# Optimization experiments

Measured on AMD Instinct MI355X. Metric: run time of the kernel, lower is better.

## Reference

```python
import jax, jax.numpy as jnp
import numpy as np

N, E, IN_DIM, HID, OUT, H = 50000, 800000, 128, 96, 96, 4
C1, C2 = HID // H, OUT // H
EPS = 1e-5

def _lin(key, out_f, in_f):
    kw, kb = jax.random.split(key)
    s = 1.0 / np.sqrt(in_f)
    W = jax.random.uniform(kw, (out_f, in_f), jnp.float32, -s, s)
    b = jax.random.uniform(kb, (out_f,), jnp.float32, -s, s)
    return W, b

def setup_inputs() -> dict:
    key = jax.random.key(0)
    ks = jax.random.split(key, 16)
    x = jax.random.normal(ks[0], (N, IN_DIM), jnp.float32)
    edge_index = jax.random.randint(ks[1], (2, E), 0, N, jnp.int64)
    Wq1, bq1 = _lin(ks[2], HID, IN_DIM)
    Wk1, bk1 = _lin(ks[3], HID, IN_DIM)
    Wv1, bv1 = _lin(ks[4], HID, IN_DIM)
    Ws1, bs1 = _lin(ks[5], HID, IN_DIM)
    Wb1 = _lin(ks[6], 1, 3 * HID)[0]
    Wq2, bq2 = _lin(ks[7], OUT, HID)
    Wk2, bk2 = _lin(ks[8], OUT, HID)
    Wv2, bv2 = _lin(ks[9], OUT, HID)
    Ws2, bs2 = _lin(ks[10], OUT, HID)
    Wb2 = _lin(ks[11], 1, 3 * OUT)[0]
    gamma = jnp.ones((OUT,), jnp.float32)
    beta = jnp.zeros((OUT,), jnp.float32)
    return dict(x=x, edge_index=edge_index, Wq1=Wq1, bq1=bq1, Wk1=Wk1, bk1=bk1,
                Wv1=Wv1, bv1=bv1, Ws1=Ws1, bs1=bs1, Wb1=Wb1,
                Wq2=Wq2, bq2=bq2, Wk2=Wk2, bk2=bk2, Wv2=Wv2, bv2=bv2,
                Ws2=Ws2, bs2=bs2, Wb2=Wb2, gamma=gamma, beta=beta)

def transformer_conv(x, src, dst, Wq, bq, Wk, bk, Wv, bv, Ws, bs, Wb, heads, ch):
    n = x.shape[0]
    q = (x @ Wq.T + bq).reshape(n, heads, ch)
    k = (x @ Wk.T + bk).reshape(n, heads, ch)
    v = (x @ Wv.T + bv).reshape(n, heads, ch)
    # per-edge attention logits [E, H]
    alpha = jnp.einsum('ehc,ehc->eh', q[dst], k[src]) / jnp.sqrt(jnp.float32(ch))
    amax = jax.ops.segment_max(alpha, dst, num_segments=n)
    a = jnp.exp(alpha - amax[dst])
    denom = jax.ops.segment_sum(a, dst, num_segments=n)
    a = a / denom[dst]
    msg = v[src] * a[:, :, None]                       # [E, H, C]
    out = jax.ops.segment_sum(msg, dst, num_segments=n).reshape(n, heads * ch)
    x_r = x @ Ws.T + bs                                # root/skip transform
    g = jax.nn.sigmoid(jnp.concatenate([out, x_r, out - x_r], -1) @ Wb.T)
    return g * x_r + (1.0 - g) * out

def reference(x, edge_index, Wq1, bq1, Wk1, bk1, Wv1, bv1, Ws1, bs1, Wb1,
              Wq2, bq2, Wk2, bk2, Wv2, bv2, Ws2, bs2, Wb2, gamma, beta):
    src, dst = edge_index[0], edge_index[1]
    h = transformer_conv(x, src, dst, Wq1, bq1, Wk1, bk1, Wv1, bv1, Ws1, bs1, Wb1, H, C1)
    h = jax.nn.gelu(h, approximate=False)
    h = transformer_conv(h, src, dst, Wq2, bq2, Wk2, bk2, Wv2, bv2, Ws2, bs2, Wb2, H, C2)
    mu = jnp.mean(h, axis=-1, keepdims=True)
    var = jnp.mean(jnp.square(h - mu), axis=-1, keepdims=True)
    return (h - mu) / jnp.sqrt(var + EPS) * gamma + beta
```

## Files before the change

kernel.cpp:

```cpp
#include <hip/hip_runtime.h>
#include <hip/hip_bf16.h>
#include <hip/hip_fp16.h>
#include <math.h>

constexpr int NN = 50000;
constexpr int EE = 800000;
constexpr int SCAN_NB = (NN + 255) / 256;

typedef short v8s __attribute__((ext_vector_type(8)));
typedef float v4f __attribute__((ext_vector_type(4)));

__device__ __forceinline__ short f2b(float f){
  __hip_bfloat16 h = __float2bfloat16(f);
  return *reinterpret_cast<short*>(&h);
}
__device__ __forceinline__ __half2 u2h2(unsigned int u){
  union { unsigned int u; __half2 h; } c; c.u = u; return c.h;
}

__global__ void hist_kernel(const int* __restrict__ ei, int* __restrict__ deg){
  int e = blockIdx.x * blockDim.x + threadIdx.x;
  if (e < EE) atomicAdd(&deg[ei[EE + e] << 4], 1);
}

__global__ __launch_bounds__(256) void partial_sum_kernel(const int* __restrict__ deg,
                                                          int* __restrict__ psum){
  int b = blockIdx.x, tid = threadIdx.x, lane = tid & 63, wv = tid >> 6;
  int i = b * 256 + tid;
  int v = (i < NN) ? deg[i << 4] : 0;
  #pragma unroll
  for (int m = 1; m < 64; m <<= 1) v += __shfl_xor(v, m);
  __shared__ int ws[4];
  if (lane == 0) ws[wv] = v;
  __syncthreads();
  if (tid == 0) psum[b] = ws[0] + ws[1] + ws[2] + ws[3];
}

__global__ __launch_bounds__(256) void scan_partials_kernel(int* __restrict__ psum){
  int tid = threadIdx.x, lane = tid & 63, wv = tid >> 6;
  int own = (tid < SCAN_NB) ? psum[tid] : 0;
  int v = own;
  #pragma unroll
  for (int off = 1; off < 64; off <<= 1){
    int t = __shfl_up(v, off);
    if (lane >= off) v += t;
  }
  __shared__ int ws[4];
  if (lane == 63) ws[wv] = v;
  __syncthreads();
  int add = 0;
  #pragma unroll
  for (int w = 0; w < 4; w++) if (w < wv) add += ws[w];
  if (tid < SCAN_NB) psum[tid] = v + add - own;
}

__global__ __launch_bounds__(256) void final_scan_kernel(const int* __restrict__ deg,
                                                         const int* __restrict__ psum,
                                                         int* __restrict__ row_ptr,
                                                         int* __restrict__ cursor){
  int b = blockIdx.x, tid = threadIdx.x, lane = tid & 63, wv = tid >> 6;
  int i = b * 256 + tid;
  int d = (i < NN) ? deg[i << 4] : 0;
  int v = d;
  #pragma unroll
  for (int off = 1; off < 64; off <<= 1){
    int t = __shfl_up(v, off);
    if (lane >= off) v += t;
  }
  __shared__ int ws[4];
  if (lane == 63) ws[wv] = v;
  __syncthreads();
  int add = psum[b];
  #pragma unroll
  for (int w = 0; w < 4; w++) if (w < wv) add += ws[w];
  if (i < NN){
    row_ptr[i + 1] = add + v;
    cursor[i << 4] = add + v - d;
  }
  if (i == 0) row_ptr[0] = 0;
}

__global__ void fill_kernel(const int* __restrict__ ei, int* __restrict__ cursor,
                            unsigned short* __restrict__ col_src){
  int e = blockIdx.x * blockDim.x + threadIdx.x;
  if (e < EE){
    int src = ei[e], dst = ei[EE + e];
    int pos = atomicAdd(&cursor[dst << 4], 1);
    col_src[pos] = (unsigned short)src;
  }
}

__global__ void pack_kernel(
    const float* __restrict__ Wq1, const float* __restrict__ bq1,
    const float* __restrict__ Wk1, const float* __restrict__ bk1,
    const float* __restrict__ Wv1, const float* __restrict__ bv1,
    const float* __restrict__ Ws1, const float* __restrict__ bs1,
    const float* __restrict__ Wq2, const float* __restrict__ bq2,
    const float* __restrict__ Wk2, const float* __restrict__ bk2,
    const float* __restrict__ Wv2, const float* __restrict__ bv2,
    const float* __restrict__ Ws2, const float* __restrict__ bs2,
    short* __restrict__ Wcat1, float* __restrict__ bcat1,
    short* __restrict__ Wcat2, float* __restrict__ bcat2){
  int c = blockIdx.x;
  int layer = c / 384, cc = c % 384;
  int which = cc / 96, r = cc % 96;
  const float* Wsel;
  const float* bsel;
  int K;
  short* Wd;
  float* bd;
  if (layer == 0){
    Wsel = which == 0 ? Wq1 : which == 1 ? Wk1 : which == 2 ? Wv1 : Ws1;
    bsel = which == 0 ? bq1 : which == 1 ? bk1 : which == 2 ? bv1 : bs1;
    K = 128; Wd = Wcat1; bd = bcat1;
  } else {
    Wsel = which == 0 ? Wq2 : which == 1 ? Wk2 : which == 2 ? Wv2 : Ws2;
    bsel = which == 0 ? bq2 : which == 1 ? bk2 : which == 2 ? bv2 : bs2;
    K = 96; Wd = Wcat2; bd = bcat2;
  }
  for (int k = threadIdx.x; k < K; k += blockDim.x)
    Wd[(size_t)cc * K + k] = f2b(Wsel[(size_t)r * K + k]);
  if (threadIdx.x == 0) bd[cc] = bsel[r];
}

template<int K, bool AF32>
__global__ __launch_bounds__(256) void gemm_kernel(const void* __restrict__ Ain,
                                                   const short* __restrict__ Wcat,
                                                   const float* __restrict__ bcat,
                                                   __half* __restrict__ qsh,
                                                   __half* __restrict__ kvb,
                                                   int M){
  constexpr int NK = K / 32;
  const int tid = threadIdx.x;
  const int lane = tid & 63, wid = tid >> 6;
  const int tile = blockIdx.x * 4 + wid;
  if (tile * 16 >= M) return;
  const int rt = tile * 16;
  const int fr = lane & 15, fk = lane >> 4;
  const int arow = rt + fr;

  v8s a[NK];
  if constexpr (AF32){
    const float* A = (const float*)Ain;
    #pragma unroll
    for (int ks = 0; ks < NK; ks++){
      const float* p = A + (size_t)arow * K + ks * 32 + fk * 8;
      float4 a0 = *(const float4*)p;
      float4 a1 = *(const float4*)(p + 4);
      v8s o;
      o[0] = f2b(a0.x); o[1] = f2b(a0.y); o[2] = f2b(a0.z); o[3] = f2b(a0.w);
      o[4] = f2b(a1.x); o[5] = f2b(a1.y); o[6] = f2b(a1.z); o[7] = f2b(a1.w);
      a[ks] = o;
    }
  } else {
    const short* A = (const short*)Ain;
    #pragma unroll
    for (int ks = 0; ks < NK; ks++)
      a[ks] = *(const v8s*)(A + (size_t)arow * K + ks * 32 + fk * 8);
  }

  #pragma unroll 4
  for (int p = 0; p < 24; p++){
    const int c0 = p * 16;
    const int gcol = c0 + fr;
    v4f acc = (v4f){0.f, 0.f, 0.f, 0.f};
    #pragma unroll
    for (int ks = 0; ks < NK; ks++){
      v8s b = *(const v8s*)(Wcat + (size_t)gcol * K + ks * 32 + fk * 8);
      acc = __builtin_amdgcn_mfma_f32_16x16x32_bf16(a[ks], b, acc, 0, 0, 0);
    }
    const float bias = bcat[gcol];
    if (c0 < 96){
      #pragma unroll
      for (int r = 0; r < 4; r++)
        qsh[(size_t)(rt + fk * 4 + r) * 192 + gcol] = __float2half(acc[r] + bias);
    } else if (c0 < 192){
      #pragma unroll
      for (int r = 0; r < 4; r++)
        kvb[(size_t)(rt + fk * 4 + r) * 192 + (gcol - 96)] = __float2half(acc[r] + bias);
    } else if (c0 < 288){
      #pragma unroll
      for (int r = 0; r < 4; r++)
        kvb[(size_t)(rt + fk * 4 + r) * 192 + 96 + (gcol - 192)] = __float2half(acc[r] + bias);
    } else {
      #pragma unroll
      for (int r = 0; r < 4; r++)
        qsh[(size_t)(rt + fk * 4 + r) * 192 + 96 + (gcol - 288)] = __float2half(acc[r] + bias);
    }
  }
}

__global__ __launch_bounds__(256) void attn_kernel(
    const __half* __restrict__ qs, const __half* __restrict__ kv,
    const int* __restrict__ row_ptr, const unsigned short* __restrict__ col_src,
    const float* __restrict__ Wb, const float* __restrict__ gamma,
    const float* __restrict__ beta, float* __restrict__ outp,
    short* __restrict__ h1b, int mode){
  const int lane = threadIdx.x & 63;
  const int wid  = threadIdx.x >> 6;
  const int n = blockIdx.x * 4 + wid;
  if (n >= NN) return;
  const int h_a = lane & 3;
  const int g_a = lane >> 2;
  const int l_v = lane & 15;
  const int vg  = lane >> 4;
  const int h_v = l_v >> 2;
  const char* kvc = (const char*)kv;
  const char* qsc = (const char*)qs;

  __half2 qh[12];
  {
    const uint4* qp = (const uint4*)(qsc + (size_t)n * 384 + h_a * 48);
    uint4 a0 = qp[0], a1 = qp[1], a2 = qp[2];
    qh[0] = u2h2(a0.x); qh[1] = u2h2(a0.y); qh[2]  = u2h2(a0.z); qh[3]  = u2h2(a0.w);
    qh[4] = u2h2(a1.x); qh[5] = u2h2(a1.y); qh[6]  = u2h2(a1.z); qh[7]  = u2h2(a1.w);
    qh[8] = u2h2(a2.x); qh[9] = u2h2(a2.y); qh[10] = u2h2(a2.z); qh[11] = u2h2(a2.w);
  }
  const int rs = row_ptr[n], re = row_ptr[n + 1];
  float m = -INFINITY, s = 0.f;
  float acc[6] = {0.f, 0.f, 0.f, 0.f, 0.f, 0.f};

  if (re > rs){
    int srcv = col_src[rs + min(g_a, re - rs - 1)];
    for (int cb = rs; cb < re; cb += 16){
      const int cn = re - cb;
      const int srcv_cur = srcv;
      if (cb + 16 < re)
        srcv = col_src[cb + 16 + min(g_a, re - cb - 17)];
      int sb[4];
      #pragma unroll
      for (int st = 0; st < 4; st++)
        sb[st] = __shfl(srcv_cur, 4 * min(st * 4 + vg, cn - 1));
      unsigned int vd[4][3];
      #pragma unroll
      for (int st = 0; st < 4; st++){
        const unsigned int* vp =
          (const unsigned int*)(kvc + (size_t)sb[st] * 384 + 192 + 12 * l_v);
        vd[st][0] = vp[0]; vd[st][1] = vp[1]; vd[st][2] = vp[2];
      }
      const uint4* kp = (const uint4*)(kvc + (size_t)srcv_cur * 384 + h_a * 48);
      uint4 u0 = kp[0], u1 = kp[1], u2 = kp[2];
      __half2 d0 = __floats2half2_rn(0.f, 0.f), d1 = d0;
      d0 = __hfma2(qh[0],  u2h2(u0.x), d0); d1 = __hfma2(qh[1],  u2h2(u0.y), d1);
      d0 = __hfma2(qh[2],  u2h2(u0.z), d0); d1 = __hfma2(qh[3],  u2h2(u0.w), d1);
      d0 = __hfma2(qh[4],  u2h2(u1.x), d0); d1 = __hfma2(qh[5],  u2h2(u1.y), d1);
      d0 = __hfma2(qh[6],  u2h2(u1.z), d0); d1 = __hfma2(qh[7],  u2h2(u1.w), d1);
      d0 = __hfma2(qh[8],  u2h2(u2.x), d0); d1 = __hfma2(qh[9],  u2h2(u2.y), d1);
      d0 = __hfma2(qh[10], u2h2(u2.z), d0); d1 = __hfma2(qh[11], u2h2(u2.w), d1);
      float dot = __low2float(d0) + __high2float(d0) + __low2float(d1) + __high2float(d1);
      float al = (g_a < cn) ? dot * 0.2041241452319315f : -INFINITY;

      float cm = al;
      cm = fmaxf(cm, __shfl_xor(cm, 4));
      cm = fmaxf(cm, __shfl_xor(cm, 8));
      cm = fmaxf(cm, __shfl_xor(cm, 16));
      cm = fmaxf(cm, __shfl_xor(cm, 32));
      float nm = fmaxf(m, cm);
      float r  = __expf(m - nm);
      float e  = __expf(al - nm);
      float cs = e;
      cs += __shfl_xor(cs, 4);
      cs += __shfl_xor(cs, 8);
      cs += __shfl_xor(cs, 16);
      cs += __shfl_xor(cs, 32);
      s = s * r + cs;
      m = nm;

      float rv = __shfl(r, h_v);
      __half2 ch0 = __floats2half2_rn(0.f, 0.f), ch1 = ch0, ch2 = ch0;
      #pragma unroll
      for (int st = 0; st < 4; st++){
        int eidx = st * 4 + vg;
        float w = __shfl(e, 4 * min(eidx, cn - 1) + h_v);
        if (eidx >= cn) w = 0.f;
        __half2 w2 = __float2half2_rn(w);
        ch0 = __hfma2(w2, u2h2(vd[st][0]), ch0);
        ch1 = __hfma2(w2, u2h2(vd[st][1]), ch1);
        ch2 = __hfma2(w2, u2h2(vd[st][2]), ch2);
      }
      acc[0] = fmaf(acc[0], rv, __low2float(ch0));
      acc[1] = fmaf(acc[1], rv, __high2float(ch0));
      acc[2] = fmaf(acc[2], rv, __low2float(ch1));
      acc[3] = fmaf(acc[3], rv, __high2float(ch1));
      acc[4] = fmaf(acc[4], rv, __low2float(ch2));
      acc[5] = fmaf(acc[5], rv, __high2float(ch2));
    }
  }

  #pragma unroll
  for (int i = 0; i < 6; i++){
    acc[i] += __shfl_xor(acc[i], 16);
    acc[i] += __shfl_xor(acc[i], 32);
  }
  float sv  = __shfl(s, h_v);
  float inv = (re > rs) ? 1.0f / sv : 0.f;
  float o[6], xr[6];
  #pragma unroll
  for (int i = 0; i < 6; i++) o[i] = acc[i] * inv;
  {
    const unsigned int* xp = (const unsigned int*)(qsc + (size_t)n * 384 + 192 + 12 * l_v);
    unsigned int x0 = xp[0], x1 = xp[1], x2 = xp[2];
    xr[0] = __low2float(u2h2(x0)); xr[1] = __high2float(u2h2(x0));
    xr[2] = __low2float(u2h2(x1)); xr[3] = __high2float(u2h2(x1));
    xr[4] = __low2float(u2h2(x2)); xr[5] = __high2float(u2h2(x2));
  }

  float p = 0.f;
  #pragma unroll
  for (int i = 0; i < 6; i++){
    int f = 6 * l_v + i;
    p += Wb[f] * o[i] + Wb[96 + f] * xr[i] + Wb[192 + f] * (o[i] - xr[i]);
  }
  p += __shfl_xor(p, 1);
  p += __shfl_xor(p, 2);
  p += __shfl_xor(p, 4);
  p += __shfl_xor(p, 8);
  float g = 1.0f / (1.0f + __expf(-p));
  float y[6];
  #pragma unroll
  for (int i = 0; i < 6; i++) y[i] = g * xr[i] + (1.0f - g) * o[i];

  if (mode == 0){
    #pragma unroll
    for (int i = 0; i < 6; i++)
      y[i] = 0.5f * y[i] * (1.0f + erff(y[i] * 0.7071067811865475f));
    if (vg == 0){
      short* op = h1b + (size_t)n * 96 + 6 * l_v;
      #pragma unroll
      for (int i = 0; i < 6; i++) op[i] = f2b(y[i]);
    }
  } else {
    float ssum = y[0] + y[1] + y[2] + y[3] + y[4] + y[5];
    ssum += __shfl_xor(ssum, 1);
    ssum += __shfl_xor(ssum, 2);
    ssum += __shfl_xor(ssum, 4);
    ssum += __shfl_xor(ssum, 8);
    float mu = ssum * (1.0f / 96.0f);
    float vsum = 0.f;
    #pragma unroll
    for (int i = 0; i < 6; i++){ float d = y[i] - mu; vsum += d * d; }
    vsum += __shfl_xor(vsum, 1);
    vsum += __shfl_xor(vsum, 2);
    vsum += __shfl_xor(vsum, 4);
    vsum += __shfl_xor(vsum, 8);
    float invs = rsqrtf(vsum * (1.0f / 96.0f) + 1e-5f);
    if (vg == 0){
      float* op = outp + (size_t)n * 96 + 6 * l_v;
      #pragma unroll
      for (int i = 0; i < 6; i++){
        int f = 6 * l_v + i;
        op[i] = (y[i] - mu) * invs * gamma[f] + beta[f];
      }
    }
  }
}

extern "C" void kernel_launch(void* const* d_in, const int* in_sizes, int n_in,
                              void* d_out, int out_size, void* d_ws, size_t ws_size,
                              hipStream_t stream){
  const float* x    = (const float*)d_in[0];
  const int*   ei   = (const int*)d_in[1];
  const float* Wq1  = (const float*)d_in[2];
  const float* bq1  = (const float*)d_in[3];
  const float* Wk1  = (const float*)d_in[4];
  const float* bk1  = (const float*)d_in[5];
  const float* Wv1  = (const float*)d_in[6];
  const float* bv1  = (const float*)d_in[7];
  const float* Ws1  = (const float*)d_in[8];
  const float* bs1  = (const float*)d_in[9];
  const float* Wb1  = (const float*)d_in[10];
  const float* Wq2  = (const float*)d_in[11];
  const float* bq2  = (const float*)d_in[12];
  const float* Wk2  = (const float*)d_in[13];
  const float* bk2  = (const float*)d_in[14];
  const float* Wv2  = (const float*)d_in[15];
  const float* bv2  = (const float*)d_in[16];
  const float* Ws2  = (const float*)d_in[17];
  const float* bs2  = (const float*)d_in[18];
  const float* Wb2  = (const float*)d_in[19];
  const float* gamma = (const float*)d_in[20];
  const float* beta  = (const float*)d_in[21];
  float* out = (float*)d_out;

  char* ws = (char*)d_ws;
  size_t off = 0;
  auto take = [&](size_t b) -> void* {
    void* p = ws + off;
    off += (b + 255) & ~(size_t)255;
    return p;
  };
  __half* qs           = (__half*)take((size_t)NN * 192 * 2);
  __half* kvb          = (__half*)take((size_t)NN * 192 * 2);
  short* h1b           = (short*)take((size_t)NN * 96 * 2);
  short* Wcat1         = (short*)take((size_t)384 * 128 * 2);
  short* Wcat2         = (short*)take((size_t)384 * 96 * 2);
  float* bcat1         = (float*)take(384 * 4);
  float* bcat2         = (float*)take(384 * 4);
  int* deg             = (int*)take((size_t)NN * 64);
  int* cursor          = (int*)take((size_t)NN * 64);
  int* row_ptr         = (int*)take((size_t)(NN + 1) * 4);
  unsigned short* col_src = (unsigned short*)take((size_t)EE * 2);
  int* psum            = (int*)take((size_t)SCAN_NB * 4);

  hipMemsetAsync(deg, 0, (size_t)NN * 64, stream);
  hist_kernel<<<(EE + 255) / 256, 256, 0, stream>>>(ei, deg);
  partial_sum_kernel<<<SCAN_NB, 256, 0, stream>>>(deg, psum);
  scan_partials_kernel<<<1, 256, 0, stream>>>(psum);
  final_scan_kernel<<<SCAN_NB, 256, 0, stream>>>(deg, psum, row_ptr, cursor);
  fill_kernel<<<(EE + 255) / 256, 256, 0, stream>>>(ei, cursor, col_src);

  pack_kernel<<<768, 128, 0, stream>>>(Wq1, bq1, Wk1, bk1, Wv1, bv1, Ws1, bs1,
                                       Wq2, bq2, Wk2, bk2, Wv2, bv2, Ws2, bs2,
                                       Wcat1, bcat1, Wcat2, bcat2);

  const int gemm_grid = ((NN + 15) / 16 + 3) / 4;
  gemm_kernel<128, true><<<gemm_grid, 256, 0, stream>>>(x, Wcat1, bcat1, qs, kvb, NN);
  attn_kernel<<<(NN + 3) / 4, 256, 0, stream>>>(qs, kvb, row_ptr, col_src, Wb1,
                                                nullptr, nullptr, nullptr, h1b, 0);
  gemm_kernel<96, false><<<gemm_grid, 256, 0, stream>>>(h1b, Wcat2, bcat2, qs, kvb, NN);
  attn_kernel<<<(NN + 3) / 4, 256, 0, stream>>>(qs, kvb, row_ptr, col_src, Wb2,
                                                gamma, beta, out, nullptr, 1);
}
```

Baseline: 289.7 us.

## Fuse hist with weight pack and CSR fill with first GEMM

Merges the degree histogram with weight packing into one launch, and the CSR fill with the layer-1 QKV GEMM into another, using block-index dispatch so the independent work runs concurrently and fewer kernels are launched. Gate weights are algebraically folded into two 96-vectors (wa = W0+W2, wc = W1-W2), cutting the gate dot product to two FMAs per element. The attention loop drops its col_src prefetch in favour of a simpler per-chunk load, which may expose more latency on the index read.

```diff
diff --git a/kernel.cpp b/kernel.cpp
--- a/kernel.cpp
+++ b/kernel.cpp
@@ -6,6 +6,9 @@
 constexpr int NN = 50000;
 constexpr int EE = 800000;
 constexpr int SCAN_NB = (NN + 255) / 256;
+constexpr int HISTB   = (EE + 255) / 256;
+constexpr int FILLB   = (EE + 255) / 256;
+constexpr int GEMMB   = ((NN + 15) / 16 + 3) / 4;
 
 typedef short v8s __attribute__((ext_vector_type(8)));
 typedef float v4f __attribute__((ext_vector_type(4)));
@@ -18,9 +21,54 @@
   union { unsigned int u; __half2 h; } c; c.u = u; return c.h;
 }
 
-__global__ void hist_kernel(const int* __restrict__ ei, int* __restrict__ deg){
-  int e = blockIdx.x * blockDim.x + threadIdx.x;
-  if (e < EE) atomicAdd(&deg[ei[EE + e] << 4], 1);
+__global__ __launch_bounds__(256) void histpack_kernel(
+    const int* __restrict__ ei, int* __restrict__ deg,
+    const float* __restrict__ Wq1, const float* __restrict__ bq1,
+    const float* __restrict__ Wk1, const float* __restrict__ bk1,
+    const float* __restrict__ Wv1, const float* __restrict__ bv1,
+    const float* __restrict__ Ws1, const float* __restrict__ bs1,
+    const float* __restrict__ Wq2, const float* __restrict__ bq2,
+    const float* __restrict__ Wk2, const float* __restrict__ bk2,
+    const float* __restrict__ Wv2, const float* __restrict__ bv2,
+    const float* __restrict__ Ws2, const float* __restrict__ bs2,
+    const float* __restrict__ Wb1, const float* __restrict__ Wb2,
+    short* __restrict__ Wcat1, float* __restrict__ bcat1,
+    short* __restrict__ Wcat2, float* __restrict__ bcat2,
+    float* __restrict__ wa1, float* __restrict__ wc1,
+    float* __restrict__ wa2, float* __restrict__ wc2){
+  int b = blockIdx.x;
+  if (b < HISTB){
+    int e = b * 256 + threadIdx.x;
+    if (e < EE) atomicAdd(&deg[ei[EE + e] << 4], 1);
+  } else if (b < HISTB + 768){
+    int c = b - HISTB;
+    int layer = c / 384, cc = c % 384;
+    int which = cc / 96, r = cc % 96;
+    const float *Wsel, *bsel;
+    int K; short* Wd; float* bd;
+    if (layer == 0){
+      Wsel = which == 0 ? Wq1 : which == 1 ? Wk1 : which == 2 ? Wv1 : Ws1;
+      bsel = which == 0 ? bq1 : which == 1 ? bk1 : which == 2 ? bv1 : bs1;
+      K = 128; Wd = Wcat1; bd = bcat1;
+    } else {
+      Wsel = which == 0 ? Wq2 : which == 1 ? Wk2 : which == 2 ? Wv2 : Ws2;
+      bsel = which == 0 ? bq2 : which == 1 ? bk2 : which == 2 ? bv2 : bs2;
+      K = 96; Wd = Wcat2; bd = bcat2;
+    }
+    for (int k = threadIdx.x; k < K; k += blockDim.x)
+      Wd[(size_t)cc * K + k] = f2b(Wsel[(size_t)r * K + k]);
+    if (threadIdx.x == 0) bd[cc] = bsel[r];
+  } else {
+    int t = threadIdx.x;
+    if (t < 96){
+      wa1[t] = Wb1[t] + Wb1[192 + t];
+      wc1[t] = Wb1[96 + t] - Wb1[192 + t];
+    } else if (t < 192){
+      int f = t - 96;
+      wa2[f] = Wb2[f] + Wb2[192 + f];
+      wc2[f] = Wb2[96 + f] - Wb2[192 + f];
+    }
+  }
 }
 
 __global__ __launch_bounds__(256) void partial_sum_kernel(const int* __restrict__ deg,
@@ -80,61 +128,15 @@
   if (i == 0) row_ptr[0] = 0;
 }
 
-__global__ void fill_kernel(const int* __restrict__ ei, int* __restrict__ cursor,
-                            unsigned short* __restrict__ col_src){
-  int e = blockIdx.x * blockDim.x + threadIdx.x;
-  if (e < EE){
-    int src = ei[e], dst = ei[EE + e];
-    int pos = atomicAdd(&cursor[dst << 4], 1);
-    col_src[pos] = (unsigned short)src;
-  }
-}
-
-__global__ void pack_kernel(
-    const float* __restrict__ Wq1, const float* __restrict__ bq1,
-    const float* __restrict__ Wk1, const float* __restrict__ bk1,
-    const float* __restrict__ Wv1, const float* __restrict__ bv1,
-    const float* __restrict__ Ws1, const float* __restrict__ bs1,
-    const float* __restrict__ Wq2, const float* __restrict__ bq2,
-    const float* __restrict__ Wk2, const float* __restrict__ bk2,
-    const float* __restrict__ Wv2, const float* __restrict__ bv2,
-    const float* __restrict__ Ws2, const float* __restrict__ bs2,
-    short* __restrict__ Wcat1, float* __restrict__ bcat1,
-    short* __restrict__ Wcat2, float* __restrict__ bcat2){
-  int c = blockIdx.x;
-  int layer = c / 384, cc = c % 384;
-  int which = cc / 96, r = cc % 96;
-  const float* Wsel;
-  const float* bsel;
-  int K;
-  short* Wd;
-  float* bd;
-  if (layer == 0){
-    Wsel = which == 0 ? Wq1 : which == 1 ? Wk1 : which == 2 ? Wv1 : Ws1;
-    bsel = which == 0 ? bq1 : which == 1 ? bk1 : which == 2 ? bv1 : bs1;
-    K = 128; Wd = Wcat1; bd = bcat1;
-  } else {
-    Wsel = which == 0 ? Wq2 : which == 1 ? Wk2 : which == 2 ? Wv2 : Ws2;
-    bsel = which == 0 ? bq2 : which == 1 ? bk2 : which == 2 ? bv2 : bs2;
-    K = 96; Wd = Wcat2; bd = bcat2;
-  }
-  for (int k = threadIdx.x; k < K; k += blockDim.x)
-    Wd[(size_t)cc * K + k] = f2b(Wsel[(size_t)r * K + k]);
-  if (threadIdx.x == 0) bd[cc] = bsel[r];
-}
-
 template<int K, bool AF32>
-__global__ __launch_bounds__(256) void gemm_kernel(const void* __restrict__ Ain,
-                                                   const short* __restrict__ Wcat,
-                                                   const float* __restrict__ bcat,
-                                                   __half* __restrict__ qsh,
-                                                   __half* __restrict__ kvb,
-                                                   int M){
+__device__ __forceinline__ void gemm_body(int tile, const void* __restrict__ Ain,
+                                          const short* __restrict__ Wcat,
+                                          const float* __restrict__ bcat,
+                                          __half* __restrict__ qsh,
+                                          __half* __restrict__ kvb, int M){
   constexpr int NK = K / 32;
-  const int tid = threadIdx.x;
-  const int lane = tid & 63, wid = tid >> 6;
-  const int tile = blockIdx.x * 4 + wid;
   if (tile * 16 >= M) return;
+  const int lane = threadIdx.x & 63;
   const int rt = tile * 16;
   const int fr = lane & 15, fk = lane >> 4;
   const int arow = rt + fr;
@@ -190,12 +192,43 @@
   }
 }
 
+template<int K, bool AF32>
+__global__ __launch_bounds__(256) void fillgemm_kernel(
+    const int* __restrict__ ei, int* __restrict__ cursor,
+    unsigned short* __restrict__ col_src,
+    const void* __restrict__ Ain, const short* __restrict__ Wcat,
+    const float* __restrict__ bcat, __half* __restrict__ qsh,
+    __half* __restrict__ kvb, int M){
+  int b = blockIdx.x;
+  if (b < FILLB){
+    int e = b * 256 + threadIdx.x;
+    if (e < EE){
+      int src = ei[e], dst = ei[EE + e];
+      int pos = atomicAdd(&cursor[dst << 4], 1);
+      col_src[pos] = (unsigned short)src;
+    }
+  } else {
+    int tile = (b - FILLB) * 4 + (threadIdx.x >> 6);
+    gemm_body<K, AF32>(tile, Ain, Wcat, bcat, qsh, kvb, M);
+  }
+}
+
+template<int K, bool AF32>
+__global__ __launch_bounds__(256) void gemm_kernel(const void* __restrict__ Ain,
+                                                   const short* __restrict__ Wcat,
+                                                   const float* __restrict__ bcat,
+                                                   __half* __restrict__ qsh,
+                                                   __half* __restrict__ kvb, int M){
+  int tile = blockIdx.x * 4 + (threadIdx.x >> 6);
+  gemm_body<K, AF32>(tile, Ain, Wcat, bcat, qsh, kvb, M);
+}
+
 __global__ __launch_bounds__(256) void attn_kernel(
     const __half* __restrict__ qs, const __half* __restrict__ kv,
     const int* __restrict__ row_ptr, const unsigned short* __restrict__ col_src,
-    const float* __restrict__ Wb, const float* __restrict__ gamma,
-    const float* __restrict__ beta, float* __restrict__ outp,
-    short* __restrict__ h1b, int mode){
+    const float* __restrict__ wa, const float* __restrict__ wc,
+    const float* __restrict__ gamma, const float* __restrict__ beta,
+    float* __restrict__ outp, short* __restrict__ h1b, int mode){
   const int lane = threadIdx.x & 63;
   const int wid  = threadIdx.x >> 6;
   const int n = blockIdx.x * 4 + wid;
@@ -220,71 +253,66 @@
   float m = -INFINITY, s = 0.f;
   float acc[6] = {0.f, 0.f, 0.f, 0.f, 0.f, 0.f};
 
-  if (re > rs){
-    int srcv = col_src[rs + min(g_a, re - rs - 1)];
-    for (int cb = rs; cb < re; cb += 16){
-      const int cn = re - cb;
-      const int srcv_cur = srcv;
-      if (cb + 16 < re)
-        srcv = col_src[cb + 16 + min(g_a, re - cb - 17)];
-      int sb[4];
-      #pragma unroll
-      for (int st = 0; st < 4; st++)
-        sb[st] = __shfl(srcv_cur, 4 * min(st * 4 + vg, cn - 1));
-      unsigned int vd[4][3];
-      #pragma unroll
-      for (int st = 0; st < 4; st++){
-        const unsigned int* vp =
-          (const unsigned int*)(kvc + (size_t)sb[st] * 384 + 192 + 12 * l_v);
-        vd[st][0] = vp[0]; vd[st][1] = vp[1]; vd[st][2] = vp[2];
-      }
-      const uint4* kp = (const uint4*)(kvc + (size_t)srcv_cur * 384 + h_a * 48);
-      uint4 u0 = kp[0], u1 = kp[1], u2 = kp[2];
-      __half2 d0 = __floats2half2_rn(0.f, 0.f), d1 = d0;
-      d0 = __hfma2(qh[0],  u2h2(u0.x), d0); d1 = __hfma2(qh[1],  u2h2(u0.y), d1);
-      d0 = __hfma2(qh[2],  u2h2(u0.z), d0); d1 = __hfma2(qh[3],  u2h2(u0.w), d1);
-      d0 = __hfma2(qh[4],  u2h2(u1.x), d0); d1 = __hfma2(qh[5],  u2h2(u1.y), d1);
-      d0 = __hfma2(qh[6],  u2h2(u1.z), d0); d1 = __hfma2(qh[7],  u2h2(u1.w), d1);
-      d0 = __hfma2(qh[8],  u2h2(u2.x), d0); d1 = __hfma2(qh[9],  u2h2(u2.y), d1);
-      d0 = __hfma2(qh[10], u2h2(u2.z), d0); d1 = __hfma2(qh[11], u2h2(u2.w), d1);
-      float dot = __low2float(d0) + __high2float(d0) + __low2float(d1) + __high2float(d1);
-      float al = (g_a < cn) ? dot * 0.2041241452319315f : -INFINITY;
-
-      float cm = al;
-      cm = fmaxf(cm, __shfl_xor(cm, 4));
-      cm = fmaxf(cm, __shfl_xor(cm, 8));
-      cm = fmaxf(cm, __shfl_xor(cm, 16));
-      cm = fmaxf(cm, __shfl_xor(cm, 32));
-      float nm = fmaxf(m, cm);
-      float r  = __expf(m - nm);
-      float e  = __expf(al - nm);
-      float cs = e;
-      cs += __shfl_xor(cs, 4);
-      cs += __shfl_xor(cs, 8);
-      cs += __shfl_xor(cs, 16);
-      cs += __shfl_xor(cs, 32);
-      s = s * r + cs;
-      m = nm;
-
-      float rv = __shfl(r, h_v);
-      __half2 ch0 = __floats2half2_rn(0.f, 0.f), ch1 = ch0, ch2 = ch0;
-      #pragma unroll
-      for (int st = 0; st < 4; st++){
-        int eidx = st * 4 + vg;
-        float w = __shfl(e, 4 * min(eidx, cn - 1) + h_v);
-        if (eidx >= cn) w = 0.f;
-        __half2 w2 = __float2half2_rn(w);
-        ch0 = __hfma2(w2, u2h2(vd[st][0]), ch0);
-        ch1 = __hfma2(w2, u2h2(vd[st][1]), ch1);
-        ch2 = __hfma2(w2, u2h2(vd[st][2]), ch2);
-      }
-      acc[0] = fmaf(acc[0], rv, __low2float(ch0));
-      acc[1] = fmaf(acc[1], rv, __high2float(ch0));
-      acc[2] = fmaf(acc[2], rv, __low2float(ch1));
-      acc[3] = fmaf(acc[3], rv, __high2float(ch1));
-      acc[4] = fmaf(acc[4], rv, __low2float(ch2));
-      acc[5] = fmaf(acc[5], rv, __high2float(ch2));
-    }
+  for (int cb = rs; cb < re; cb += 16){
+    const int cn = re - cb;
+    int srcv = col_src[cb + min(g_a, cn - 1)];
+    int sb[4];
+    #pragma unroll
+    for (int st = 0; st < 4; st++)
+      sb[st] = __shfl(srcv, 4 * min(st * 4 + vg, cn - 1));
+    unsigned int vd[4][3];
+    #pragma unroll
+    for (int st = 0; st < 4; st++){
+      const unsigned int* vp =
+        (const unsigned int*)(kvc + (size_t)sb[st] * 384 + 192 + 12 * l_v);
+      vd[st][0] = vp[0]; vd[st][1] = vp[1]; vd[st][2] = vp[2];
+    }
+    const uint4* kp = (const uint4*)(kvc + (size_t)srcv * 384 + h_a * 48);
+    uint4 u0 = kp[0], u1 = kp[1], u2 = kp[2];
+    __half2 d0 = __floats2half2_rn(0.f, 0.f), d1 = d0;
+    d0 = __hfma2(qh[0],  u2h2(u0.x), d0); d1 = __hfma2(qh[1],  u2h2(u0.y), d1);
+    d0 = __hfma2(qh[2],  u2h2(u0.z), d0); d1 = __hfma2(qh[3],  u2h2(u0.w), d1);
+    d0 = __hfma2(qh[4],  u2h2(u1.x), d0); d1 = __hfma2(qh[5],  u2h2(u1.y), d1);
+    d0 = __hfma2(qh[6],  u2h2(u1.z), d0); d1 = __hfma2(qh[7],  u2h2(u1.w), d1);
+    d0 = __hfma2(qh[8],  u2h2(u2.x), d0); d1 = __hfma2(qh[9],  u2h2(u2.y), d1);
+    d0 = __hfma2(qh[10], u2h2(u2.z), d0); d1 = __hfma2(qh[11], u2h2(u2.w), d1);
+    float dot = __low2float(d0) + __high2float(d0) + __low2float(d1) + __high2float(d1);
+    float al = (g_a < cn) ? dot * 0.2041241452319315f : -INFINITY;
+
+    float cm = al;
+    cm = fmaxf(cm, __shfl_xor(cm, 4));
+    cm = fmaxf(cm, __shfl_xor(cm, 8));
+    cm = fmaxf(cm, __shfl_xor(cm, 16));
+    cm = fmaxf(cm, __shfl_xor(cm, 32));
+    float nm = fmaxf(m, cm);
+    float r  = __expf(m - nm);
+    float e  = __expf(al - nm);
+    float cs = e;
+    cs += __shfl_xor(cs, 4);
+    cs += __shfl_xor(cs, 8);
+    cs += __shfl_xor(cs, 16);
+    cs += __shfl_xor(cs, 32);
+    s = s * r + cs;
+    m = nm;
+
+    float rv = __shfl(r, h_v);
+    __half2 ch0 = __floats2half2_rn(0.f, 0.f), ch1 = ch0, ch2 = ch0;
+    #pragma unroll
+    for (int st = 0; st < 4; st++){
+      int eidx = st * 4 + vg;
+      float w = __shfl(e, 4 * min(eidx, cn - 1) + h_v);
+      if (eidx >= cn) w = 0.f;
+      __half2 w2 = __float2half2_rn(w);
+      ch0 = __hfma2(w2, u2h2(vd[st][0]), ch0);
+      ch1 = __hfma2(w2, u2h2(vd[st][1]), ch1);
+      ch2 = __hfma2(w2, u2h2(vd[st][2]), ch2);
+    }
+    acc[0] = fmaf(acc[0], rv, __low2float(ch0));
+    acc[1] = fmaf(acc[1], rv, __high2float(ch0));
+    acc[2] = fmaf(acc[2], rv, __low2float(ch1));
+    acc[3] = fmaf(acc[3], rv, __high2float(ch1));
+    acc[4] = fmaf(acc[4], rv, __low2float(ch2));
+    acc[5] = fmaf(acc[5], rv, __high2float(ch2));
   }
 
   #pragma unroll
@@ -309,7 +337,8 @@
   #pragma unroll
   for (int i = 0; i < 6; i++){
     int f = 6 * l_v + i;
-    p += Wb[f] * o[i] + Wb[96 + f] * xr[i] + Wb[192 + f] * (o[i] - xr[i]);
+    p = fmaf(o[i], wa[f], p);
+    p = fmaf(xr[i], wc[f], p);
   }
   p += __shfl_xor(p, 1);
   p += __shfl_xor(p, 2);
@@ -318,7 +347,7 @@
   float g = 1.0f / (1.0f + __expf(-p));
   float y[6];
   #pragma unroll
-  for (int i = 0; i < 6; i++) y[i] = g * xr[i] + (1.0f - g) * o[i];
+  for (int i = 0; i < 6; i++) y[i] = fmaf(g, xr[i] - o[i], o[i]);
 
   if (mode == 0){
     #pragma unroll
@@ -396,6 +425,10 @@
   short* Wcat2         = (short*)take((size_t)384 * 96 * 2);
   float* bcat1         = (float*)take(384 * 4);
   float* bcat2         = (float*)take(384 * 4);
+  float* wa1           = (float*)take(96 * 4);
+  float* wc1           = (float*)take(96 * 4);
+  float* wa2           = (float*)take(96 * 4);
+  float* wc2           = (float*)take(96 * 4);
   int* deg             = (int*)take((size_t)NN * 64);
   int* cursor          = (int*)take((size_t)NN * 64);
   int* row_ptr         = (int*)take((size_t)(NN + 1) * 4);
@@ -403,21 +436,22 @@
   int* psum            = (int*)take((size_t)SCAN_NB * 4);
 
   hipMemsetAsync(deg, 0, (size_t)NN * 64, stream);
-  hist_kernel<<<(EE + 255) / 256, 256, 0, stream>>>(ei, deg);
+  histpack_kernel<<<HISTB + 768 + 1, 256, 0, stream>>>(
+      ei, deg,
+      Wq1, bq1, Wk1, bk1, Wv1, bv1, Ws1, bs1,
+      Wq2, bq2, Wk2, bk2, Wv2, bv2, Ws2, bs2,
+      Wb1, Wb2, Wcat1, bcat1, Wcat2, bcat2, wa1, wc1, wa2, wc2);
   partial_sum_kernel<<<SCAN_NB, 256, 0, stream>>>(deg, psum);
   scan_partials_kernel<<<1, 256, 0, stream>>>(psum);
   final_scan_kernel<<<SCAN_NB, 256, 0, stream>>>(deg, psum, row_ptr, cursor);
-  fill_kernel<<<(EE + 255) / 256, 256, 0, stream>>>(ei, cursor, col_src);
-
-  pack_kernel<<<768, 128, 0, stream>>>(Wq1, bq1, Wk1, bk1, Wv1, bv1, Ws1, bs1,
-                                       Wq2, bq2, Wk2, bk2, Wv2, bv2, Ws2, bs2,
-                                       Wcat1, bcat1, Wcat2, bcat2);
-
-  const int gemm_grid = ((NN + 15) / 16 + 3) / 4;
-  gemm_kernel<128, true><<<gemm_grid, 256, 0, stream>>>(x, Wcat1, bcat1, qs, kvb, NN);
-  attn_kernel<<<(NN + 3) / 4, 256, 0, stream>>>(qs, kvb, row_ptr, col_src, Wb1,
-                                                nullptr, nullptr, nullptr, h1b, 0);
-  gemm_kernel<96, false><<<gemm_grid, 256, 0, stream>>>(h1b, Wcat2, bcat2, qs, kvb, NN);
-  attn_kernel<<<(NN + 3) / 4, 256, 0, stream>>>(qs, kvb, row_ptr, col_src, Wb2,
-                                                gamma, beta, out, nullptr, 1);
-}
+
+  fillgemm_kernel<128, true><<<FILLB + GEMMB, 256, 0, stream>>>(
+      ei, cursor, col_src, x, Wcat1, bcat1, qs, kvb, NN);
+  attn_kernel<<<(NN + 3) / 4, 256, 0, stream>>>(qs, kvb, row_ptr, col_src,
+                                                wa1, wc1, nullptr, nullptr,
+                                                nullptr, h1b, 0);
+  gemm_kernel<96, false><<<GEMMB, 256, 0, stream>>>(h1b, Wcat2, bcat2, qs, kvb, NN);
+  attn_kernel<<<(NN + 3) / 4, 256, 0, stream>>>(qs, kvb, row_ptr, col_src,
+                                                wa2, wc2, gamma, beta,
+                                                out, nullptr, 1);
+}
```

Result: no change. 285.0 us (-1.6%).
